# Optimization experiments

Hardware: AMD Instinct MI355X
Metric: run time of the kernel (lower is better)

The kernel has to match this reference:

```python
import math
import jax, jax.numpy as jnp
import numpy as np

H = 12   # num attention heads
DH = 64  # head dim
K = 2    # pooling kernel
ST = 2   # pooling stride


def _alibi_slopes(n):
    def pow2_slopes(n):
        start = 2 ** (-2 ** (-(math.log2(n) - 3)))
        return [start * (start ** i) for i in range(n)]
    if math.log2(n).is_integer():
        return pow2_slopes(n)
    c = 2 ** math.floor(math.log2(n))
    return pow2_slopes(c) + _alibi_slopes(2 * c)[0::2][: n - c]


def _alibi_bias(p, s):
    # [1, H, p, s]; -slope * |i - j|
    rel = np.abs(np.arange(s)[None, :] - np.arange(p)[:, None]).astype(np.float32)
    slopes = np.asarray(_alibi_slopes(H), dtype=np.float32)
    return jnp.asarray((-slopes[:, None, None] * rel[None])[None])


def masked_avg_pool(x, mask):
    # x: [b, S, d] float, mask: [b, S] bool
    b, S, d = x.shape
    pad = (K - S) if K > S else (S - K) % ST
    if pad:
        x = jnp.pad(x, ((0, 0), (0, pad), (0, 0)))
        mask = jnp.pad(mask, ((0, 0), (0, pad)))
    p = (S + pad - K) // ST + 1
    idx = jnp.arange(p)[:, None] * ST + jnp.arange(K)[None, :]  # [p, K]
    xb = x[:, idx]        # [b, p, K, d]
    mb = mask[:, idx]     # [b, p, K]
    norm = jnp.maximum(mb.sum(-1), 1).astype(x.dtype)  # [b, p]
    y = (xb * mb[..., None].astype(x.dtype)).sum(-2) / norm[..., None]
    return y, mb.any(-1)


def setup_inputs() -> dict:
    key = jax.random.key(0)
    k1, k2, k3, k4 = jax.random.split(key, 4)
    B, S, D = 64, 512, 768
    return {
        "hidden_states": jax.random.normal(k1, (B, S, D), dtype=jnp.float32),
        "attention_mask": jax.random.randint(k2, (B, S), 0, 2, dtype=jnp.int32),
        "Wqkv_w": jax.random.normal(k3, (D, 3 * D), dtype=jnp.float32) * 0.02,
        "Wqkv_b": jax.random.normal(k4, (3 * D,), dtype=jnp.float32) * 0.02,
    }


def reference(hidden_states, attention_mask, Wqkv_w, Wqkv_b):
    mask = attention_mask.astype(bool)                    # [b, s]
    b, s, _ = hidden_states.shape
    # fused QKV proj; repad() zeroes padded rows
    qkv = (hidden_states @ Wqkv_w + Wqkv_b) * mask[..., None].astype(hidden_states.dtype)
    q, k, v = jnp.split(qkv, 3, axis=-1)                  # each [b, s, H*DH]
    # masked avg pooling of queries (flattened heads, as in the module)
    q_pooled, new_mask = masked_avg_pool(q, mask)         # [b, p, H*DH], [b, p]
    p = q_pooled.shape[1]
    qh = q_pooled.reshape(b, p, H, DH).transpose(0, 2, 1, 3)  # [b, H, p, DH]
    kh = k.reshape(b, s, H, DH).transpose(0, 2, 1, 3)         # [b, H, s, DH]
    vh = v.reshape(b, s, H, DH).transpose(0, 2, 1, 3)
    # additive bias: 0 where both query and key valid, else -10000; plus ALiBi
    pair = new_mask[:, :, None] & mask[:, None, :]            # [b, p, s]
    bias = jnp.where(pair, 0.0, -10000.0)[:, None] + _alibi_bias(p, s)  # [b, H, p, s]
    scores = jnp.einsum("bhpd,bhsd->bhps", qh, kh) / math.sqrt(DH) + bias
    attn = jax.nn.softmax(scores, axis=-1)
    out = jnp.einsum("bhps,bhsd->bhpd", attn, vh)             # [b, H, p, DH]
    attn_output = out.transpose(0, 2, 1, 3).reshape(b, p, H * DH)
    nm = new_mask[..., None].astype(attn_output.dtype)
    attn_output = attn_output * nm        # emulate unpad(): zero invalid rows
    residual_query = q_pooled * nm
    return attn_output, new_mask, residual_query
```

## Files before the change

kernel.cpp:

```cpp
#include <hip/hip_runtime.h>
#include <cstdint>
#include <cstddef>

#define HH 12
#define DHD 64
#define BB 64
#define SS 512
#define DD 768
#define PP 256
#define N3 2304

typedef __attribute__((ext_vector_type(8))) short bf16x8_t;
typedef __attribute__((ext_vector_type(4))) float f32x4_t;

__constant__ float c_slopes[12] = {
  0.5f, 0.25f, 0.125f, 0.0625f, 0.03125f, 0.015625f, 0.0078125f, 0.00390625f,
  0.70710678118654752f, 0.35355339059327376f, 0.17677669529663688f, 0.08838834764831844f
};

__device__ __forceinline__ ushort f2bf(float f) {
  union { float f; unsigned u; } v; v.f = f;
  unsigned r = v.u + 0x7fffu + ((v.u >> 16) & 1u);
  return (ushort)(r >> 16);
}
__device__ __forceinline__ float bf2f(ushort u) {
  union { unsigned u; float f; } v; v.u = ((unsigned)u) << 16;
  return v.f;
}
__device__ __forceinline__ void gload_lds16(const ushort* g, ushort* l) {
  __builtin_amdgcn_global_load_lds(
      (const __attribute__((address_space(1))) void*)g,
      (__attribute__((address_space(3))) void*)l, 16, 0, 0);
}

__global__ __launch_bounds__(256) void prep_kernel(
    const float* __restrict__ hs, const int* __restrict__ mask,
    ushort* __restrict__ A, ushort* __restrict__ Ap,
    const float* __restrict__ W, ushort* __restrict__ Wt,
    float* __restrict__ nmask_out) {
  if (blockIdx.x < 8192) {
    const int row0 = blockIdx.x * 4;
    const int t = threadIdx.x;
    if (t < 192) {
      float4 v[4];
#pragma unroll
      for (int r = 0; r < 4; r++) {
        v[r] = ((const float4*)hs)[(size_t)(row0 + r) * 192 + t];
        ushort4 o;
        o.x = f2bf(v[r].x); o.y = f2bf(v[r].y); o.z = f2bf(v[r].z); o.w = f2bf(v[r].w);
        ((ushort4*)A)[(size_t)(row0 + r) * 192 + t] = o;
      }
      const int m0 = mask[row0], m1 = mask[row0 + 1];
      const int m2 = mask[row0 + 2], m3 = mask[row0 + 3];
      const float f0 = (float)m0, f1 = (float)m1, f2 = (float)m2, f3 = (float)m3;
      const float inv0 = 1.0f / (float)((m0 + m1) < 1 ? 1 : (m0 + m1));
      const float inv1 = 1.0f / (float)((m2 + m3) < 1 ? 1 : (m2 + m3));
      ushort4 p0, p1;
      p0.x = f2bf((f0 * v[0].x + f1 * v[1].x) * inv0);
      p0.y = f2bf((f0 * v[0].y + f1 * v[1].y) * inv0);
      p0.z = f2bf((f0 * v[0].z + f1 * v[1].z) * inv0);
      p0.w = f2bf((f0 * v[0].w + f1 * v[1].w) * inv0);
      p1.x = f2bf((f2 * v[2].x + f3 * v[3].x) * inv1);
      p1.y = f2bf((f2 * v[2].y + f3 * v[3].y) * inv1);
      p1.z = f2bf((f2 * v[2].z + f3 * v[3].z) * inv1);
      p1.w = f2bf((f2 * v[2].w + f3 * v[3].w) * inv1);
      const int prow = row0 >> 1;
      ((ushort4*)Ap)[(size_t)prow * 192 + t]       = p0;
      ((ushort4*)Ap)[(size_t)(prow + 1) * 192 + t] = p1;
      if (t == 0) {
        nmask_out[prow]     = (m0 + m1) > 0 ? 1.0f : 0.0f;
        nmask_out[prow + 1] = (m2 + m3) > 0 ? 1.0f : 0.0f;
      }
    }
  } else {
    __shared__ float tile[32][33];
    int tb = blockIdx.x - 8192;
    int n0 = (tb % 72) * 32, k0 = (tb / 72) * 32;
    int tx = threadIdx.x & 31, ty = threadIdx.x >> 5;
    for (int r = ty; r < 32; r += 8) tile[r][tx] = W[(size_t)(k0 + r) * N3 + n0 + tx];
    __syncthreads();
    for (int r = ty; r < 32; r += 8) Wt[(size_t)(n0 + r) * DD + k0 + tx] = f2bf(tile[tx][r]);
  }
}

__global__ __launch_bounds__(512, 2) void gemm_qkv_kernel(
    const ushort* __restrict__ A, const ushort* __restrict__ Ap,
    const ushort* __restrict__ Wt, const float* __restrict__ bias,
    const int* __restrict__ mask, const float* __restrict__ nmask,
    ushort* __restrict__ Kbuf, ushort* __restrict__ Vbuf,
    float* __restrict__ resid, ushort* __restrict__ qp) {
  __shared__ __align__(16) ushort As[2][16384];
  __shared__ __align__(16) ushort Bs[2][16384];
  const int wg = blockIdx.x;
  const int swz = (wg & 7) * 120 + (wg >> 3);
  int bm, wtb; const ushort* Asrc; bool isQ;
  if (swz < 768) { isQ = false; bm = (swz / 6) * 256; wtb = 768 + (swz % 6) * 256; Asrc = A; }
  else { isQ = true; int q = swz - 768; bm = (q / 3) * 256; wtb = (q % 3) * 256; Asrc = Ap; }
  const int tid = threadIdx.x;
  const int lane = tid & 63;
  const int wave = tid >> 6;
  const int wm = (wave >> 2) * 128;
  const int wn = (wave & 3) * 64;
  const int fr = lane & 15, quad = lane >> 4;
  const int xr = (fr & 7) << 3;
  const int q8 = quad * 8;

  const int rsub = tid >> 3;
  const int cg8 = ((tid & 7) ^ (rsub & 7)) * 8;
  const ushort* Ag = Asrc + (size_t)(bm + rsub) * DD + cg8;
  const ushort* Bg = Wt + (size_t)(wtb + rsub) * DD + cg8;
  ushort* AsW = &As[0][0] + wave * 512;
  ushort* BsW = &Bs[0][0] + wave * 512;

  f32x4_t acc[8][4];
#pragma unroll
  for (int i = 0; i < 8; i++)
#pragma unroll
    for (int j = 0; j < 4; j++) acc[i][j] = (f32x4_t){0.f, 0.f, 0.f, 0.f};

#pragma unroll
  for (int l = 0; l < 4; l++) {
    gload_lds16(Ag + (size_t)l * 64 * DD,      AsW + l * 4096);
    gload_lds16(Bg + (size_t)l * 64 * DD,      BsW + l * 4096);
  }
#pragma unroll
  for (int l = 0; l < 4; l++) {
    gload_lds16(Ag + (size_t)l * 64 * DD + 64, AsW + 16384 + l * 4096);
    gload_lds16(Bg + (size_t)l * 64 * DD + 64, BsW + 16384 + l * 4096);
  }
  asm volatile("s_waitcnt vmcnt(8)" ::: "memory");
  __builtin_amdgcn_s_barrier();
  asm volatile("" ::: "memory");

#pragma unroll 2
  for (int t = 0; t < 12; t++) {
    const ushort* Ab = &As[t & 1][0];
    const ushort* Bb = &Bs[t & 1][0];
    bf16x8_t a[4][2], b[4][2];
#pragma unroll
    for (int m = 0; m < 4; m++)
#pragma unroll
      for (int kk = 0; kk < 2; kk++)
        a[m][kk] = *(const bf16x8_t*)&Ab[(wm + m * 16 + fr) * 64 + ((kk * 32 + q8) ^ xr)];
#pragma unroll
    for (int n = 0; n < 4; n++)
#pragma unroll
      for (int kk = 0; kk < 2; kk++)
        b[n][kk] = *(const bf16x8_t*)&Bb[(wn + n * 16 + fr) * 64 + ((kk * 32 + q8) ^ xr)];
#pragma unroll
    for (int m = 0; m < 4; m++)
#pragma unroll
      for (int n = 0; n < 4; n++) {
        acc[m][n] = __builtin_amdgcn_mfma_f32_16x16x32_bf16(a[m][0], b[n][0], acc[m][n], 0, 0, 0);
        acc[m][n] = __builtin_amdgcn_mfma_f32_16x16x32_bf16(a[m][1], b[n][1], acc[m][n], 0, 0, 0);
      }
#pragma unroll
    for (int m = 0; m < 4; m++)
#pragma unroll
      for (int kk = 0; kk < 2; kk++)
        a[m][kk] = *(const bf16x8_t*)&Ab[(wm + 64 + m * 16 + fr) * 64 + ((kk * 32 + q8) ^ xr)];
#pragma unroll
    for (int m = 0; m < 4; m++)
#pragma unroll
      for (int n = 0; n < 4; n++) {
        acc[4 + m][n] = __builtin_amdgcn_mfma_f32_16x16x32_bf16(a[m][0], b[n][0], acc[4 + m][n], 0, 0, 0);
        acc[4 + m][n] = __builtin_amdgcn_mfma_f32_16x16x32_bf16(a[m][1], b[n][1], acc[4 + m][n], 0, 0, 0);
      }
    asm volatile("s_waitcnt lgkmcnt(0)" ::: "memory");
    __builtin_amdgcn_sched_barrier(0);
    __builtin_amdgcn_s_barrier();
    if (t < 10) {
      const size_t koff = (size_t)(t + 2) * 64;
      ushort* Ad = AsW + (t & 1) * 16384;
      ushort* Bd = BsW + (t & 1) * 16384;
#pragma unroll
      for (int l = 0; l < 4; l++) {
        gload_lds16(Ag + (size_t)l * 64 * DD + koff, Ad + l * 4096);
        gload_lds16(Bg + (size_t)l * 64 * DD + koff, Bd + l * 4096);
      }
      asm volatile("s_waitcnt vmcnt(8)" ::: "memory");
    } else {
      asm volatile("s_waitcnt vmcnt(0)" ::: "memory");
    }
    __builtin_amdgcn_s_barrier();
    asm volatile("" ::: "memory");
  }

  float bb[4];
#pragma unroll
  for (int j = 0; j < 4; j++) bb[j] = bias[wtb + wn + j * 16 + fr];
  if (!isQ) {
    ushort* dst = (wtb < 1536) ? Kbuf : Vbuf;
    const int cb = (wtb < 1536) ? (wtb - 768) : (wtb - 1536);
#pragma unroll
    for (int i = 0; i < 8; i++) {
      const int gm = bm + wm + i * 16 + quad * 4;
#pragma unroll
      for (int r = 0; r < 4; r++) {
        const float mv = (float)mask[gm + r];
        ushort* orow = dst + (size_t)(gm + r) * DD + cb + wn + fr;
#pragma unroll
        for (int j = 0; j < 4; j++)
          orow[j * 16] = f2bf((acc[i][j][r] + bb[j]) * mv);
      }
    }
  } else {
#pragma unroll
    for (int i = 0; i < 8; i++) {
      const int gm = bm + wm + i * 16 + quad * 4;
#pragma unroll
      for (int r = 0; r < 4; r++) {
        const float qm = nmask[gm + r];
        float* rrow = resid + (size_t)(gm + r) * DD + wtb + wn + fr;
        ushort* qrow = qp + (size_t)(gm + r) * DD + wtb + wn + fr;
#pragma unroll
        for (int j = 0; j < 4; j++) {
          float v = acc[i][j][r] + bb[j] * qm;
          rrow[j * 16] = v;
          qrow[j * 16] = f2bf(v * 0.125f);
        }
      }
    }
  }
}

__global__ __launch_bounds__(512, 2) void attn_kernel(
    const ushort* __restrict__ Kbuf, const ushort* __restrict__ Vbuf,
    const ushort* __restrict__ qp,
    const int* __restrict__ mask, const float* __restrict__ nmask,
    float* __restrict__ outA) {
  __shared__ __align__(16) ushort K_lds[512 * 64];
  __shared__ __align__(16) ushort VT_lds[64 * 512];
  __shared__ __align__(16) ushort P_lds[8][32][40];
  __shared__ __align__(16) float  kb[512];
  const int h = blockIdx.x, b = blockIdx.y;
  const int tid = threadIdx.x, wave = tid >> 6, lane = tid & 63;
  const int fr = lane & 15, quad = lane >> 4;
  const int kxor = (fr & 7) << 4;
  const float slope = c_slopes[h];

  {
    const int r0 = lane >> 3;
    const int cg = ((lane & 7) ^ r0) * 8;
    const ushort* Ks = Kbuf + (size_t)(b * 512 + wave * 64 + r0) * DD + h * 64 + cg;
#pragma unroll
    for (int i = 0; i < 8; i++)
      gload_lds16(Ks + (size_t)i * 8 * DD, K_lds + (wave * 64 + i * 8) * 64);
  }
  {
    const ushort* Vs = Vbuf + (size_t)(b * 512 + tid) * DD + h * 64;
    float4 vr[8];
#pragma unroll
    for (int d0 = 0; d0 < 8; d0++) vr[d0] = *(const float4*)(Vs + d0 * 8);
    const int s2 = tid * 2;
    const int sbase = (s2 & ~15), slo = (s2 & 15);
#pragma unroll
    for (int d0 = 0; d0 < 8; d0++) {
      ushort tmp[8];
      *(float4*)tmp = vr[d0];
#pragma unroll
      for (int j = 0; j < 8; j++) {
        int d = d0 * 8 + j;
        *(ushort*)((char*)VT_lds + (size_t)d * 1024 + ((sbase ^ ((d & 7) << 4)) + slo)) = tmp[j];
      }
    }
  }
  kb[tid] = mask[b * 512 + tid] ? 0.0f : -10000.0f;
  bf16x8_t qf[2][2];
#pragma unroll
  for (int nt = 0; nt < 2; nt++)
#pragma unroll
    for (int ks = 0; ks < 2; ks++)
      qf[nt][ks] = *(const bf16x8_t*)(qp + (size_t)(b * 256 + wave * 32 + nt * 16 + fr) * 768
                                      + h * 64 + ks * 32 + quad * 8);
  __syncthreads();

  const char* Kc = (const char*)K_lds;
  const char* Vc = (const char*)VT_lds;
  char* Pw = (char*)&P_lds[wave][0][0];

  f32x4_t O[2][4];
#pragma unroll
  for (int i = 0; i < 2; i++)
#pragma unroll
    for (int j = 0; j < 4; j++) O[i][j] = (f32x4_t){0.f, 0.f, 0.f, 0.f};
  float m_run[2] = {-3.0e38f, -3.0e38f};
  float l_run[2] = {0.f, 0.f};

  for (int sb = 0; sb < 512; sb += 64) {
    f32x4_t sacc[4][2];
#pragma unroll
    for (int mt = 0; mt < 4; mt++) { sacc[mt][0] = (f32x4_t){0,0,0,0}; sacc[mt][1] = (f32x4_t){0,0,0,0}; }
#pragma unroll
    for (int ks = 0; ks < 2; ks++)
#pragma unroll
      for (int mt = 0; mt < 4; mt++) {
        bf16x8_t ak = *(const bf16x8_t*)(Kc + (size_t)(sb + mt * 16 + fr) * 128
                                         + ((ks * 64 + quad * 16) ^ kxor));
        sacc[mt][0] = __builtin_amdgcn_mfma_f32_16x16x32_bf16(ak, qf[0][ks], sacc[mt][0], 0, 0, 0);
        sacc[mt][1] = __builtin_amdgcn_mfma_f32_16x16x32_bf16(ak, qf[1][ks], sacc[mt][1], 0, 0, 0);
      }
    float kbv[4][4];
#pragma unroll
    for (int mt = 0; mt < 4; mt++) {
      f32x4_t kv = *(const f32x4_t*)&kb[sb + mt * 16 + quad * 4];
#pragma unroll
      for (int r = 0; r < 4; r++) kbv[mt][r] = kv[r];
    }
    float pv2[2][4][4];
    float fsv[2];
#pragma unroll
    for (int nt = 0; nt < 2; nt++) {
      const float pidx = (float)(wave * 32 + nt * 16 + fr);
      float mx = -3.0e38f;
#pragma unroll
      for (int mt = 0; mt < 4; mt++)
#pragma unroll
        for (int r = 0; r < 4; r++) {
          float s_ = (float)(sb + mt * 16 + quad * 4 + r);
          float v = sacc[mt][nt][r] + kbv[mt][r] - slope * fabsf(s_ - pidx);
          pv2[nt][mt][r] = v;
          mx = fmaxf(mx, v);
        }
      mx = fmaxf(mx, __shfl_xor(mx, 16, 64));
      mx = fmaxf(mx, __shfl_xor(mx, 32, 64));
      float mnew = fmaxf(m_run[nt], mx);
      float f = __expf(m_run[nt] - mnew);
      m_run[nt] = mnew; fsv[nt] = f;
      float rs = 0.f;
#pragma unroll
      for (int mt = 0; mt < 4; mt++)
#pragma unroll
        for (int r = 0; r < 4; r++) {
          float e = __expf(pv2[nt][mt][r] - mnew);
          pv2[nt][mt][r] = e; rs += e;
        }
      rs += __shfl_xor(rs, 16, 64);
      rs += __shfl_xor(rs, 32, 64);
      l_run[nt] = l_run[nt] * f + rs;
    }
#pragma unroll
    for (int mp = 0; mp < 2; mp++)
#pragma unroll
      for (int r = 0; r < 4; r++) {
        float fb = __shfl(fsv[mp], quad * 4 + r, 64);
#pragma unroll
        for (int nd = 0; nd < 4; nd++) O[mp][nd][r] *= fb;
      }
#pragma unroll
    for (int c = 0; c < 2; c++) {
#pragma unroll
      for (int nt = 0; nt < 2; nt++)
#pragma unroll
        for (int mm = 0; mm < 2; mm++) {
          int mt = c * 2 + mm;
          ushort4 pk;
          pk.x = f2bf(pv2[nt][mt][0]); pk.y = f2bf(pv2[nt][mt][1]);
          pk.z = f2bf(pv2[nt][mt][2]); pk.w = f2bf(pv2[nt][mt][3]);
          *(ushort4*)(Pw + (nt * 16 + fr) * 80 + mm * 32 + quad * 8) = pk;
        }
      bf16x8_t ap0 = *(const bf16x8_t*)(Pw + fr * 80 + quad * 16);
      bf16x8_t ap1 = *(const bf16x8_t*)(Pw + (16 + fr) * 80 + quad * 16);
#pragma unroll
      for (int nd = 0; nd < 4; nd++) {
        bf16x8_t bv = *(const bf16x8_t*)(Vc + (size_t)(nd * 16 + fr) * 1024
                                         + (((sb + c * 32) * 2 + quad * 16) ^ kxor));
        O[0][nd] = __builtin_amdgcn_mfma_f32_16x16x32_bf16(ap0, bv, O[0][nd], 0, 0, 0);
        O[1][nd] = __builtin_amdgcn_mfma_f32_16x16x32_bf16(ap1, bv, O[1][nd], 0, 0, 0);
      }
    }
  }

#pragma unroll
  for (int mp = 0; mp < 2; mp++) {
    const int p0 = wave * 32 + mp * 16 + quad * 4;
#pragma unroll
    for (int r = 0; r < 4; r++) {
      float lb = __shfl(l_run[mp], quad * 4 + r, 64);
      float nm = nmask[b * 256 + p0 + r];
      float scl = nm / lb;
#pragma unroll
      for (int nd = 0; nd < 4; nd++)
        outA[(size_t)(b * 256 + p0 + r) * 768 + h * 64 + nd * 16 + fr] = O[mp][nd][r] * scl;
    }
  }
}

extern "C" void kernel_launch(void* const* d_in, const int* in_sizes, int n_in,
                              void* d_out, int out_size, void* d_ws, size_t ws_size,
                              hipStream_t stream) {
  const float* hs   = (const float*)d_in[0];
  const int*   mask = (const int*)d_in[1];
  const float* W    = (const float*)d_in[2];
  const float* bias = (const float*)d_in[3];
  float* out = (float*)d_out;
  char* ws = (char*)d_ws;
  ushort* A    = (ushort*)(ws);
  ushort* Wt   = (ushort*)(ws + 50331648);
  ushort* Kbuf = (ushort*)(ws + 53870592);
  ushort* Vbuf = (ushort*)(ws + 104202240);
  ushort* Ap   = (ushort*)(ws + 154533888);
  ushort* qp   = (ushort*)(ws + 179699712);
  float* nmask = out + 12582912;
  float* resid = out + 12599296;

  hipLaunchKernelGGL(prep_kernel, dim3(9920), dim3(256), 0, stream,
                     hs, mask, A, Ap, W, Wt, nmask);
  hipLaunchKernelGGL(gemm_qkv_kernel, dim3(960), dim3(512), 0, stream,
                     A, Ap, Wt, bias, mask, nmask, Kbuf, Vbuf, resid, qp);
  hipLaunchKernelGGL(attn_kernel, dim3(12, 64), dim3(512), 0, stream,
                     Kbuf, Vbuf, qp, mask, nmask, out);
}
```

Baseline: 389.8 us.

## Interleave QKV GEMM global-to-LDS loads with MFMA in eight-phase ping-pong schedule

Restructures the QKV projection GEMM main loop into eight sub-phases per two K-tiles. Each phase issues a slice of the next tile's global-to-LDS loads, reads a quarter of the fragments, and runs a quarter of the MFMAs, with barriers and s_setprio raised around the math. This spreads memory traffic across the compute instead of issuing it in one burst, hiding load latency in the style of HipKittens 8-wave ping-pong. In exchange it adds many more barriers, and the vmcnt accounting is finer-grained and easier to get wrong.

```diff
diff --git a/kernel.cpp b/kernel.cpp
--- a/kernel.cpp
+++ b/kernel.cpp
@@ -111,6 +111,40 @@
   const ushort* Bg = Wt + (size_t)(wtb + rsub) * DD + cg8;
   ushort* AsW = &As[0][0] + wave * 512;
   ushort* BsW = &Bs[0][0] + wave * 512;
+  const ushort* A0 = &As[0][0]; const ushort* B0 = &Bs[0][0];
+  const ushort* A1 = &As[1][0]; const ushort* B1 = &Bs[1][0];
+
+#define ST_A(tt, l0, l1) { const size_t ko = (size_t)(tt) * 64;                      \
+    ushort* d = AsW + (((tt) & 1) << 14);                                            \
+    gload_lds16(Ag + (size_t)(l0) * 64 * DD + ko, d + (l0) * 4096);                  \
+    gload_lds16(Ag + (size_t)(l1) * 64 * DD + ko, d + (l1) * 4096); }
+#define ST_B(tt, l0, l1) { const size_t ko = (size_t)(tt) * 64;                      \
+    ushort* d = BsW + (((tt) & 1) << 14);                                            \
+    gload_lds16(Bg + (size_t)(l0) * 64 * DD + ko, d + (l0) * 4096);                  \
+    gload_lds16(Bg + (size_t)(l1) * 64 * DD + ko, d + (l1) * 4096); }
+#define RD_A(dst, Ab, mh)                                                            \
+  _Pragma("unroll") for (int m = 0; m < 4; m++)                                      \
+  _Pragma("unroll") for (int kk = 0; kk < 2; kk++)                                   \
+    dst[m][kk] = *(const bf16x8_t*)&Ab[(wm + (mh) * 64 + m * 16 + fr) * 64 + ((kk * 32 + q8) ^ xr)];
+#define RD_B(dst, Bb, nh)                                                            \
+  _Pragma("unroll") for (int n = 0; n < 2; n++)                                      \
+  _Pragma("unroll") for (int kk = 0; kk < 2; kk++)                                   \
+    dst[n][kk] = *(const bf16x8_t*)&Bb[(wn + (nh) * 32 + n * 16 + fr) * 64 + ((kk * 32 + q8) ^ xr)];
+#define PH_MID                                                                        \
+    asm volatile("" ::: "memory");                                                    \
+    __builtin_amdgcn_s_barrier();                                                     \
+    asm volatile("s_waitcnt lgkmcnt(0)" ::: "memory");                                \
+    __builtin_amdgcn_sched_barrier(0);                                                \
+    __builtin_amdgcn_s_setprio(1);
+#define PH_END                                                                        \
+    __builtin_amdgcn_s_setprio(0);                                                    \
+    asm volatile("" ::: "memory");                                                    \
+    __builtin_amdgcn_s_barrier();
+#define MM(mb, nb, aa, bb_)                                                           \
+  _Pragma("unroll") for (int m = 0; m < 4; m++)                                       \
+  _Pragma("unroll") for (int n = 0; n < 2; n++) {                                     \
+    acc[(mb)+m][(nb)+n] = __builtin_amdgcn_mfma_f32_16x16x32_bf16(aa[m][0], bb_[n][0], acc[(mb)+m][(nb)+n], 0, 0, 0); \
+    acc[(mb)+m][(nb)+n] = __builtin_amdgcn_mfma_f32_16x16x32_bf16(aa[m][1], bb_[n][1], acc[(mb)+m][(nb)+n], 0, 0, 0); }
 
   f32x4_t acc[8][4];
 #pragma unroll
@@ -118,72 +152,42 @@
 #pragma unroll
     for (int j = 0; j < 4; j++) acc[i][j] = (f32x4_t){0.f, 0.f, 0.f, 0.f};
 
-#pragma unroll
-  for (int l = 0; l < 4; l++) {
-    gload_lds16(Ag + (size_t)l * 64 * DD,      AsW + l * 4096);
-    gload_lds16(Bg + (size_t)l * 64 * DD,      BsW + l * 4096);
-  }
-#pragma unroll
-  for (int l = 0; l < 4; l++) {
-    gload_lds16(Ag + (size_t)l * 64 * DD + 64, AsW + 16384 + l * 4096);
-    gload_lds16(Bg + (size_t)l * 64 * DD + 64, BsW + 16384 + l * 4096);
-  }
-  asm volatile("s_waitcnt vmcnt(8)" ::: "memory");
+  ST_A(0, 0, 1); ST_A(0, 2, 3); ST_B(0, 0, 1); ST_B(0, 2, 3);
+  ST_A(1, 0, 2); ST_B(1, 0, 1); ST_A(1, 1, 3);
+  asm volatile("s_waitcnt vmcnt(6)" ::: "memory");
   __builtin_amdgcn_s_barrier();
   asm volatile("" ::: "memory");
 
-#pragma unroll 2
-  for (int t = 0; t < 12; t++) {
-    const ushort* Ab = &As[t & 1][0];
-    const ushort* Bb = &Bs[t & 1][0];
-    bf16x8_t a[4][2], b[4][2];
-#pragma unroll
-    for (int m = 0; m < 4; m++)
-#pragma unroll
-      for (int kk = 0; kk < 2; kk++)
-        a[m][kk] = *(const bf16x8_t*)&Ab[(wm + m * 16 + fr) * 64 + ((kk * 32 + q8) ^ xr)];
-#pragma unroll
-    for (int n = 0; n < 4; n++)
-#pragma unroll
-      for (int kk = 0; kk < 2; kk++)
-        b[n][kk] = *(const bf16x8_t*)&Bb[(wn + n * 16 + fr) * 64 + ((kk * 32 + q8) ^ xr)];
-#pragma unroll
-    for (int m = 0; m < 4; m++)
-#pragma unroll
-      for (int n = 0; n < 4; n++) {
-        acc[m][n] = __builtin_amdgcn_mfma_f32_16x16x32_bf16(a[m][0], b[n][0], acc[m][n], 0, 0, 0);
-        acc[m][n] = __builtin_amdgcn_mfma_f32_16x16x32_bf16(a[m][1], b[n][1], acc[m][n], 0, 0, 0);
-      }
-#pragma unroll
-    for (int m = 0; m < 4; m++)
-#pragma unroll
-      for (int kk = 0; kk < 2; kk++)
-        a[m][kk] = *(const bf16x8_t*)&Ab[(wm + 64 + m * 16 + fr) * 64 + ((kk * 32 + q8) ^ xr)];
-#pragma unroll
-    for (int m = 0; m < 4; m++)
-#pragma unroll
-      for (int n = 0; n < 4; n++) {
-        acc[4 + m][n] = __builtin_amdgcn_mfma_f32_16x16x32_bf16(a[m][0], b[n][0], acc[4 + m][n], 0, 0, 0);
-        acc[4 + m][n] = __builtin_amdgcn_mfma_f32_16x16x32_bf16(a[m][1], b[n][1], acc[4 + m][n], 0, 0, 0);
-      }
-    asm volatile("s_waitcnt lgkmcnt(0)" ::: "memory");
-    __builtin_amdgcn_sched_barrier(0);
-    __builtin_amdgcn_s_barrier();
-    if (t < 10) {
-      const size_t koff = (size_t)(t + 2) * 64;
-      ushort* Ad = AsW + (t & 1) * 16384;
-      ushort* Bd = BsW + (t & 1) * 16384;
-#pragma unroll
-      for (int l = 0; l < 4; l++) {
-        gload_lds16(Ag + (size_t)l * 64 * DD + koff, Ad + l * 4096);
-        gload_lds16(Bg + (size_t)l * 64 * DD + koff, Bd + l * 4096);
-      }
-      asm volatile("s_waitcnt vmcnt(8)" ::: "memory");
-    } else {
-      asm volatile("s_waitcnt vmcnt(0)" ::: "memory");
-    }
-    __builtin_amdgcn_s_barrier();
-    asm volatile("" ::: "memory");
+#pragma unroll 1
+  for (int i = 0; i < 6; i++) {
+    bf16x8_t a[4][2], b0[2][2], b1[2][2];
+    const bool st = (i < 5);
+    RD_A(a, A0, 0); RD_B(b0, B0, 0);
+    ST_B(2 * i + 1, 2, 3);
+    PH_MID; MM(0, 0, a, b0); PH_END;
+    RD_B(b1, B0, 1);
+    if (st) ST_A(2 * i + 2, 0, 2);
+    PH_MID; MM(0, 2, a, b1); PH_END;
+    RD_A(a, A0, 1);
+    if (st) ST_B(2 * i + 2, 0, 1);
+    PH_MID; MM(4, 0, a, b0); PH_END;
+    if (st) { ST_A(2 * i + 2, 1, 3);
+              asm volatile("s_waitcnt vmcnt(6)" ::: "memory"); }
+    else    { asm volatile("s_waitcnt vmcnt(0)" ::: "memory"); }
+    PH_MID; MM(4, 2, a, b1); PH_END;
+    RD_A(a, A1, 0); RD_B(b0, B1, 0);
+    if (st) ST_B(2 * i + 2, 2, 3);
+    PH_MID; MM(0, 0, a, b0); PH_END;
+    RD_B(b1, B1, 1);
+    if (st) ST_A(2 * i + 3, 0, 2);
+    PH_MID; MM(0, 2, a, b1); PH_END;
+    RD_A(a, A1, 1);
+    if (st) ST_B(2 * i + 3, 0, 1);
+    PH_MID; MM(4, 0, a, b0); PH_END;
+    if (st) { ST_A(2 * i + 3, 1, 3);
+              asm volatile("s_waitcnt vmcnt(6)" ::: "memory"); }
+    else    { asm volatile("s_waitcnt vmcnt(0)" ::: "memory"); }
+    PH_MID; MM(4, 2, a, b1); PH_END;
   }
 
   float bb[4];
@@ -222,6 +226,13 @@
       }
     }
   }
+#undef ST_A
+#undef ST_B
+#undef RD_A
+#undef RD_B
+#undef PH_MID
+#undef PH_END
+#undef MM
 }
 
 __global__ __launch_bounds__(512, 2) void attn_kernel(
```

Measured after the change: 391.4 us. Within noise of the previous version (+0.4%).
